# Optimization experiments

Hardware: AMD Instinct MI355X
Metric: run time of the kernel (lower is better)

## Reference

```python
import jax, jax.numpy as jnp
import numpy as np

K = 3
STRIDE = 1
PAD = 1
GROUPS = 16
EPS = 1e-5


def _conv2d(x, w, b, stride, pad):
    out = jax.lax.conv_general_dilated(
        x, w, (stride, stride), [(pad, pad), (pad, pad)],
        dimension_numbers=("NCHW", "OIHW", "NCHW"))
    return out + b[None, :, None, None]


def setup_inputs() -> dict:
    key = jax.random.key(0)
    ks = jax.random.split(key, 6)
    B, Cin, H, W = 4, 256, 64, 64
    Cout = 256
    x = jax.random.normal(ks[0], (B, Cin, H, W), dtype=jnp.float32)
    # DCNv2 offset/mask-generating conv: 3*K*K = 27 output channels
    w_off = jax.random.normal(ks[1], (3 * K * K, Cin, K, K), dtype=jnp.float32) * 0.01
    b_off = jnp.zeros((3 * K * K,), dtype=jnp.float32)
    # main deformable conv weight/bias
    weight = jax.random.normal(ks[2], (Cout, Cin, K, K), dtype=jnp.float32) * 0.02
    bias = jnp.zeros((Cout,), dtype=jnp.float32)
    # GroupNorm affine params
    gamma = jnp.ones((Cout,), dtype=jnp.float32)
    beta = jnp.zeros((Cout,), dtype=jnp.float32)
    return {"x": x, "w_off": w_off, "b_off": b_off,
            "weight": weight, "bias": bias, "gamma": gamma, "beta": beta}


def reference(x, w_off, b_off, weight, bias, gamma, beta):
    B, Cin, H, W = x.shape
    Cout = weight.shape[0]
    KK = K * K

    # --- offset/mask branch (DCNv2): 18 offsets + 9 sigmoid masks ---
    om = _conv2d(x, w_off, b_off, STRIDE, PAD)          # [B, 27, Ho, Wo]
    Ho, Wo = om.shape[2], om.shape[3]
    off_y, off_x, m = jnp.split(om, 3, axis=1)          # each [B, 9, Ho, Wo]
    mask = jax.nn.sigmoid(m)

    # --- sampling coordinates: base grid + kernel tap + learned offset ---
    kgy = jnp.repeat(jnp.arange(K, dtype=x.dtype), K)   # [9] row of tap
    kgx = jnp.tile(jnp.arange(K, dtype=x.dtype), K)     # [9] col of tap
    base_y = jnp.arange(Ho, dtype=x.dtype) * STRIDE - PAD
    base_x = jnp.arange(Wo, dtype=x.dtype) * STRIDE - PAD
    py = base_y[None, None, :, None] + kgy[None, :, None, None] + off_y  # [B,9,Ho,Wo]
    px = base_x[None, None, None, :] + kgx[None, :, None, None] + off_x  # [B,9,Ho,Wo]

    # --- bilinear sampling with zero padding outside the image ---
    y0 = jnp.floor(py)
    x0 = jnp.floor(px)
    wy1 = py - y0
    wx1 = px - x0

    def gather(img, yy, xx):
        # img [Cin,H,W], yy/xx [9,Ho,Wo] int -> [Cin,9,Ho,Wo]
        return img[:, yy, xx]

    def corner(yi, xi, wy, wx):
        valid = (yi >= 0) & (yi < H) & (xi >= 0) & (xi < W)
        yc = jnp.clip(yi, 0, H - 1).astype(jnp.int32)
        xc = jnp.clip(xi, 0, W - 1).astype(jnp.int32)
        vals = jax.vmap(gather)(x, yc, xc)               # [B,Cin,9,Ho,Wo]
        w_ = (wy * wx * valid.astype(x.dtype))[:, None]   # [B,1,9,Ho,Wo]
        return vals * w_

    sampled = (corner(y0, x0, (1 - wy1), (1 - wx1))
               + corner(y0, x0 + 1, (1 - wy1), wx1)
               + corner(y0 + 1, x0, wy1, (1 - wx1))
               + corner(y0 + 1, x0 + 1, wy1, wx1))       # [B,Cin,9,Ho,Wo]
    sampled = sampled * mask[:, None]                     # modulation

    # --- conv accumulation over taps and input channels ---
    out = jnp.einsum("bckhw,ock->bohw", sampled,
                     weight.reshape(Cout, Cin, KK)) + bias[None, :, None, None]

    # --- GroupNorm(16, Cout) ---
    og = out.reshape(B, GROUPS, Cout // GROUPS, Ho, Wo)
    mu = og.mean(axis=(2, 3, 4), keepdims=True)
    var = og.var(axis=(2, 3, 4), keepdims=True)
    og = (og - mu) * jax.lax.rsqrt(var + EPS)
    out = og.reshape(B, Cout, Ho, Wo) * gamma[None, :, None, None] + beta[None, :, None, None]
    return out
```

## Files before the change

### kernel.cpp

```cpp
#include <hip/hip_runtime.h>
#include <math.h>

#define CIN   256
#define COUT  256
#define H     64
#define W     64
#define HW    4096
#define KK    9
#define KC    2304
#define NOFF  27
#define B_    4
#define EPS   1e-5f
#define OM3S  (B_ * NOFF * HW)

typedef __attribute__((ext_vector_type(4))) float f32x4;
typedef __attribute__((ext_vector_type(8))) short s16x8;

static __device__ __forceinline__ unsigned short f2bf(float f) {
  unsigned u = __builtin_bit_cast(unsigned, f);
  u += 0x7FFF + ((u >> 16) & 1);
  return (unsigned short)(u >> 16);
}
static __device__ __forceinline__ float bflo(unsigned u) {
  return __builtin_bit_cast(float, u << 16);
}
static __device__ __forceinline__ float bfhi(unsigned u) {
  return __builtin_bit_cast(float, u & 0xffff0000u);
}
static __device__ __forceinline__ unsigned packbf(float lo, float hi) {
  unsigned ul = __builtin_bit_cast(unsigned, lo);
  unsigned uh = __builtin_bit_cast(unsigned, hi);
  ul += 0x7FFF + ((ul >> 16) & 1);
  uh += 0x7FFF + ((uh >> 16) & 1);
  return (ul >> 16) | (uh & 0xffff0000u);
}

__global__ __launch_bounds__(256) void prep_kernel(
    const float* __restrict__ x, const float* __restrict__ w,
    const float* __restrict__ w_off, unsigned short* __restrict__ xT,
    unsigned short* __restrict__ wBf, unsigned short* __restrict__ wOBf,
    float* __restrict__ gstat) {
  int bi = blockIdx.x;
  int t = threadIdx.x;
  if (bi < 256) {
    __shared__ unsigned short tile[64][272];
    int b = bi >> 6, y = bi & 63;
    const float* src = x + (size_t)b * CIN * HW + y * W;
    for (int r = 0; r < 64; ++r) {
      int idx = r * 256 + t;
      int c = idx >> 6, ww = idx & 63;
      tile[ww][c] = f2bf(src[(size_t)c * HW + ww]);
    }
    __syncthreads();
    unsigned short* dst = xT + ((size_t)(b * 64 + y) * 64) * 256;
    for (int r = 0; r < 8; ++r) {
      int idx = r * 2048 + t * 8;
      int ww = idx >> 8, c = idx & 255;
      *(uint4*)(dst + idx) = *(const uint4*)&tile[ww][c];
    }
  } else if (bi < 544) {
    int pkt = (bi - 256) * 256 + t;
    int lane = pkt & 63;
    int tn = (pkt >> 6) & 15;
    int k2 = pkt >> 10;
    int co = tn * 16 + (lane & 15);
    int kb = k2 * 32 + (lane >> 4) * 8;
    unsigned short v[8];
#pragma unroll
    for (int j = 0; j < 8; ++j) {
      int kk = kb + j;
      int kt = kk >> 8, c = kk & 255;
      v[j] = f2bf(w[(co * 256 + c) * 9 + kt]);
    }
    *(uint4*)&wBf[(size_t)pkt * 8] = *(const uint4*)v;
  } else if (bi < 580) {
    int pkt = (bi - 544) * 256 + t;
    int lane = pkt & 63;
    int tn = (pkt >> 6) & 1;
    int k2 = pkt >> 7;
    int oc = tn * 16 + (lane & 15);
    int kb = k2 * 32 + (lane >> 4) * 8;
    unsigned short v[8];
#pragma unroll
    for (int j = 0; j < 8; ++j) {
      int kk = kb + j;
      int kt = kk >> 8, c = kk & 255;
      v[j] = (oc < NOFF) ? f2bf(w_off[(oc * 256 + c) * 9 + kt]) : (unsigned short)0;
    }
    *(uint4*)&wOBf[(size_t)pkt * 8] = *(const uint4*)v;
  } else {
    if (t < 128) gstat[t] = 0.f;
  }
}

__global__ __launch_bounds__(256) void offconv_mfma_kernel(
    const unsigned short* __restrict__ xT, const unsigned short* __restrict__ wOBf,
    float* __restrict__ om3) {
  int bi = blockIdx.x;
  int ts = bi >> 8;
  int row = bi & 255;
  int b = row >> 6, i = row & 63;
  int t = threadIdx.x, lane = t & 63, wv = t >> 6;
  int lr = lane & 15, lq = lane >> 4;
  int p = wv * 16 + lr;
  const unsigned short* xb = xT + (size_t)b * (HW * 256);
  f32x4 acc[2] = {};

  for (int kc = 0; kc < 3; ++kc) {
    int kt = ts * 3 + kc;
    int ky = kt / 3, kx = kt % 3;
    int yy = i - 1 + ky, xx = p - 1 + kx;
    bool ok = ((unsigned)yy < 64u) && ((unsigned)xx < 64u);
    const unsigned short* ap = xb + ((ok ? yy * 64 + xx : 0) << 8) + lq * 8;
#pragma unroll
    for (int c8 = 0; c8 < 8; ++c8) {
      uint4 av = uint4{0, 0, 0, 0};
      if (ok) av = *(const uint4*)(ap + c8 * 32);
      int k2 = kt * 8 + c8;
      s16x8 a = __builtin_bit_cast(s16x8, av);
      s16x8 b0 = *(const s16x8*)(wOBf + ((((k2 * 2 + 0) << 6) | lane) << 3));
      s16x8 b1 = *(const s16x8*)(wOBf + ((((k2 * 2 + 1) << 6) | lane) << 3));
      acc[0] = __builtin_amdgcn_mfma_f32_16x16x32_bf16(a, b0, acc[0], 0, 0, 0);
      acc[1] = __builtin_amdgcn_mfma_f32_16x16x32_bf16(a, b1, acc[1], 0, 0, 0);
    }
  }
#pragma unroll
  for (int tn = 0; tn < 2; ++tn) {
    int oc = tn * 16 + lr;
    if (oc < NOFF) {
      float* ob = om3 + (size_t)ts * OM3S + ((b * NOFF + oc) << 12) + i * 64 + wv * 16;
#pragma unroll
      for (int r = 0; r < 4; ++r) ob[lq * 4 + r] = acc[tn][r];
    }
  }
}

__global__ __launch_bounds__(512, 2) void gemm_fused_kernel(
    const unsigned short* __restrict__ xT, const float* __restrict__ om3,
    const float* __restrict__ b_off, const unsigned short* __restrict__ wBf,
    const float* __restrict__ bias, unsigned short* __restrict__ cvt,
    float* __restrict__ gstat) {
  __shared__ float tapw[64][KK][4];
  __shared__ int   tapc[64][KK][4];
  __shared__ unsigned short At[2][64 * 64];
  int bid = blockIdx.x;
  int mt = ((bid & 7) << 5) | (bid >> 3);
  int m0 = mt * 64;
  int b = m0 >> 12;
  int irow = (m0 & 4095) >> 6;
  int t = threadIdx.x;
  int lane = t & 63, wv = t >> 6;
  int lr = lane & 15, lq = lane >> 4;
  const unsigned short* xb = xT + (size_t)b * (HW * 256);

  for (int idx = t; idx < 64 * KK; idx += 512) {
    int p = idx / KK, k = idx % KK;
    int pix = (m0 & 4095) + p;
    size_t o = (size_t)(b * NOFF) * HW + pix;
    float offy = om3[o + k * HW] + om3[OM3S + o + k * HW] +
                 om3[2 * OM3S + o + k * HW] + b_off[k];
    float offx = om3[o + (9 + k) * HW] + om3[OM3S + o + (9 + k) * HW] +
                 om3[2 * OM3S + o + (9 + k) * HW] + b_off[9 + k];
    float mval = om3[o + (18 + k) * HW] + om3[OM3S + o + (18 + k) * HW] +
                 om3[2 * OM3S + o + (18 + k) * HW] + b_off[18 + k];
    float mask = 1.f / (1.f + __expf(-mval));
    float py = (float)(irow - 1 + k / 3) + offy;
    float px = (float)(p - 1 + k % 3) + offx;
    float y0f = floorf(py), x0f = floorf(px);
    float wy1 = py - y0f, wx1 = px - x0f;
    int y0 = (int)y0f, x0 = (int)x0f;
    bool y0ok = (unsigned)y0 < 64u, y1ok = (unsigned)(y0 + 1) < 64u;
    bool x0ok = (unsigned)x0 < 64u, x1ok = (unsigned)(x0 + 1) < 64u;
    tapw[p][k][0] = (1.f - wy1) * (1.f - wx1) * mask * (float)(y0ok && x0ok);
    tapw[p][k][1] = (1.f - wy1) * wx1 * mask * (float)(y0ok && x1ok);
    tapw[p][k][2] = wy1 * (1.f - wx1) * mask * (float)(y1ok && x0ok);
    tapw[p][k][3] = wy1 * wx1 * mask * (float)(y1ok && x1ok);
    int y0c = min(max(y0, 0), 63), y1c = min(max(y0 + 1, 0), 63);
    int x0c = min(max(x0, 0), 63), x1c = min(max(x0 + 1, 0), 63);
    tapc[p][k][0] = (y0c * 64 + x0c) * 256;
    tapc[p][k][1] = (x1c - x0c) * 256;
    tapc[p][k][2] = (y1c - y0c) * 64 * 256;
    tapc[p][k][3] = 0;
  }
  __syncthreads();

  bool isProd = (wv < 4);
  int p = (t & 255) >> 2, q = t & 3;
  int cw = isProd ? 0 : (wv - 4);
  const unsigned short* bb = wBf + ((size_t)(cw * 4) * 64 + lane) * 8;

  f32x4 acc[4][4] = {};
  s16x8 Bfa[2][4], Bfb[2][4];
  uint4 sG[8];

#define GLOAD(JJ)                                                            \
  {                                                                          \
    int kt_ = (JJ) >> 2, cg_ = (JJ) & 3;                                     \
    int4 tc_ = *(const int4*)&tapc[p][kt_][0];                               \
    const unsigned short* c_ = xb + tc_.x + cg_ * 64 + q * 16;               \
    sG[0] = *(const uint4*)(c_);                                             \
    sG[1] = *(const uint4*)(c_ + 8);                                         \
    sG[2] = *(const uint4*)(c_ + tc_.y);                                     \
    sG[3] = *(const uint4*)(c_ + tc_.y + 8);                                 \
    sG[4] = *(const uint4*)(c_ + tc_.z);                                     \
    sG[5] = *(const uint4*)(c_ + tc_.z + 8);                                 \
    sG[6] = *(const uint4*)(c_ + tc_.z + tc_.y);                             \
    sG[7] = *(const uint4*)(c_ + tc_.z + tc_.y + 8);                         \
  }

#define COMBINE(JJ, BUFI)                                                    \
  {                                                                          \
    int kt_ = (JJ) >> 2;                                                     \
    f32x4 tw_ = *(const f32x4*)&tapw[p][kt_][0];                             \
    _Pragma("unroll") for (int o = 0; o < 2; ++o) {                          \
      const unsigned* a00_ = (const unsigned*)&sG[0 + o];                    \
      const unsigned* a01_ = (const unsigned*)&sG[2 + o];                    \
      const unsigned* a10_ = (const unsigned*)&sG[4 + o];                    \
      const unsigned* a11_ = (const unsigned*)&sG[6 + o];                    \
      uint4 res_;                                                            \
      unsigned* rr_ = (unsigned*)&res_;                                      \
      _Pragma("unroll") for (int u = 0; u < 4; ++u) {                        \
        float lo_ = tw_[0] * bflo(a00_[u]) + tw_[1] * bflo(a01_[u]) +        \
                    tw_[2] * bflo(a10_[u]) + tw_[3] * bflo(a11_[u]);         \
        float hi_ = tw_[0] * bfhi(a00_[u]) + tw_[1] * bfhi(a01_[u]) +        \
                    tw_[2] * bfhi(a10_[u]) + tw_[3] * bfhi(a11_[u]);         \
        rr_[u] = packbf(lo_, hi_);                                           \
      }                                                                      \
      *(uint4*)((char*)At[BUFI] + p * 128 + (((q * 2 + o) ^ (p & 7)) * 16)) = res_; \
    }                                                                        \
  }

#define BISSUE(J, SLOT)                                                      \
  {                                                                          \
    int k2b_ = (J) * 2;                                                      \
    _Pragma("unroll") for (int kh = 0; kh < 2; ++kh)                         \
      _Pragma("unroll") for (int tn = 0; tn < 4; ++tn)                       \
        SLOT[kh][tn] = *(const s16x8*)(bb + (size_t)(k2b_ + kh) * 8192 + tn * 512); \
  }

#define CONSUME(BUFI, SLOT)                                                  \
  {                                                                          \
    const char* buf_ = (const char*)At[BUFI];                                \
    _Pragma("unroll") for (int kh = 0; kh < 2; ++kh) {                       \
      s16x8 af[4];                                                           \
      _Pragma("unroll") for (int tm = 0; tm < 4; ++tm) {                     \
        int r_ = tm * 16 + lr;                                               \
        af[tm] = *(const s16x8*)(buf_ + r_ * 128 + (((kh * 4 + lq) ^ (r_ & 7)) * 16)); \
      }                                                                      \
      __builtin_amdgcn_s_setprio(1);                                         \
      _Pragma("unroll") for (int tm = 0; tm < 4; ++tm)                       \
        _Pragma("unroll") for (int tn = 0; tn < 4; ++tn)                     \
          acc[tm][tn] = __builtin_amdgcn_mfma_f32_16x16x32_bf16(             \
              af[tm], SLOT[kh][tn], acc[tm][tn], 0, 0, 0);                   \
      __builtin_amdgcn_s_setprio(0);                                         \
    }                                                                        \
  }

#define SOFTBAR()                                                            \
  {                                                                          \
    asm volatile("s_waitcnt lgkmcnt(0)" ::: "memory");                       \
    __builtin_amdgcn_sched_barrier(0);                                       \
    __builtin_amdgcn_s_barrier();                                            \
  }

  if (isProd) {
    GLOAD(0);
    COMBINE(0, 0);
    GLOAD(1);
  } else {
    BISSUE(0, Bfa);
    BISSUE(1, Bfb);
  }
  SOFTBAR();

#pragma unroll 1
  for (int k = 0; k < 36; k += 2) {
    if (isProd) {
      COMBINE(k + 1, 1);
      if (k + 2 < 36) GLOAD(k + 2);
    } else {
      CONSUME(0, Bfa);
      if (k + 2 < 36) BISSUE(k + 2, Bfa);
    }
    SOFTBAR();
    if (isProd) {
      if (k + 2 < 36) COMBINE(k + 2, 0);
      if (k + 3 < 36) GLOAD(k + 3);
    } else {
      CONSUME(1, Bfb);
      if (k + 3 < 36) BISSUE(k + 3, Bfb);
    }
    SOFTBAR();
  }

#undef GLOAD
#undef COMBINE
#undef BISSUE
#undef CONSUME
#undef SOFTBAR

  if (!isProd) {
    int poff = m0 & 4095;
#pragma unroll
    for (int tn = 0; tn < 4; ++tn) {
      int co = cw * 64 + tn * 16 + lr;
      float bco = bias[co];
      unsigned short* cvb = cvt + (size_t)(b * COUT + co) * HW + poff;
      float sS = 0.f, qq = 0.f;
#pragma unroll
      for (int tm = 0; tm < 4; ++tm) {
        ushort4 st;
#pragma unroll
        for (int r = 0; r < 4; ++r) {
          float v = acc[tm][tn][r] + bco;
          sS += v;
          qq += v * v;
          ((unsigned short*)&st)[r] = f2bf(v);
        }
        *(ushort4*)(cvb + tm * 16 + lq * 4) = st;
      }
#pragma unroll
      for (int off = 32; off > 0; off >>= 1) {
        sS += __shfl_down(sS, off, 64);
        qq += __shfl_down(qq, off, 64);
      }
      if (lane == 0) {
        int g = co >> 4;
        atomicAdd(&gstat[(b * 16 + g) * 2 + 0], sS);
        atomicAdd(&gstat[(b * 16 + g) * 2 + 1], qq);
      }
    }
  }
}

__global__ __launch_bounds__(256) void gn_apply_kernel(
    const unsigned short* __restrict__ convout, const float* __restrict__ gstat,
    const float* __restrict__ gamma, const float* __restrict__ beta,
    float* __restrict__ out) {
  int vid = blockIdx.x * 256 + threadIdx.x;
  int e = vid * 8;
  int b = e >> 20;
  int c = (e >> 12) & 255;
  int g = c >> 4;
  float S = gstat[(b * 16 + g) * 2 + 0];
  float Q = gstat[(b * 16 + g) * 2 + 1];
  float mu = S * (1.f / 65536.f);
  float var = Q * (1.f / 65536.f) - mu * mu;
  float rs = rsqrtf(var + EPS);
  float a = rs * gamma[c];
  float bb = beta[c] - mu * a;
  uint4 v = *(const uint4*)(convout + e);
  const unsigned* u = (const unsigned*)&v;
  float4 o0, o1;
  o0.x = bflo(u[0]) * a + bb;  o0.y = bfhi(u[0]) * a + bb;
  o0.z = bflo(u[1]) * a + bb;  o0.w = bfhi(u[1]) * a + bb;
  o1.x = bflo(u[2]) * a + bb;  o1.y = bfhi(u[2]) * a + bb;
  o1.z = bflo(u[3]) * a + bb;  o1.w = bfhi(u[3]) * a + bb;
  *(float4*)(out + e) = o0;
  *(float4*)(out + e + 4) = o1;
}

extern "C" void kernel_launch(void* const* d_in, const int* in_sizes, int n_in,
                              void* d_out, int out_size, void* d_ws, size_t ws_size,
                              hipStream_t stream) {
  const float* x      = (const float*)d_in[0];
  const float* w_off  = (const float*)d_in[1];
  const float* b_off  = (const float*)d_in[2];
  const float* weight = (const float*)d_in[3];
  const float* bias   = (const float*)d_in[4];
  const float* gamma  = (const float*)d_in[5];
  const float* beta   = (const float*)d_in[6];
  float* out = (float*)d_out;

  float* om3 = (float*)d_ws;
  unsigned short* xT   = (unsigned short*)(om3 + (size_t)3 * OM3S);
  unsigned short* wBf  = xT + (size_t)B_ * HW * 256;
  unsigned short* wOBf = wBf + (size_t)COUT * KC;
  unsigned short* cvt  = wOBf + (size_t)32 * KC;
  float* gstat = (float*)(cvt + (size_t)B_ * HW * COUT);

  prep_kernel<<<dim3(581), dim3(256), 0, stream>>>(x, weight, w_off, xT, wBf, wOBf, gstat);
  offconv_mfma_kernel<<<dim3(768), dim3(256), 0, stream>>>(xT, wOBf, om3);
  gemm_fused_kernel<<<dim3(256), dim3(512), 0, stream>>>(xT, om3, b_off, wBf, bias, cvt, gstat);
  gn_apply_kernel<<<dim3(2048), dim3(256), 0, stream>>>(cvt, gstat, gamma, beta, out);
}
```

Baseline: 166.7 us.

## Fuse offset/mask conv into main deformable GEMM kernel via shared memory

```diff
diff --git a/kernel.cpp b/kernel.cpp
--- a/kernel.cpp
+++ b/kernel.cpp
@@ -11,7 +11,6 @@
 #define NOFF  27
 #define B_    4
 #define EPS   1e-5f
-#define OM3S  (B_ * NOFF * HW)
 
 typedef __attribute__((ext_vector_type(4))) float f32x4;
 typedef __attribute__((ext_vector_type(8))) short s16x8;
@@ -93,56 +92,15 @@
   }
 }
 
-__global__ __launch_bounds__(256) void offconv_mfma_kernel(
+__global__ __launch_bounds__(512, 1) void gemm_fused_kernel(
     const unsigned short* __restrict__ xT, const unsigned short* __restrict__ wOBf,
-    float* __restrict__ om3) {
-  int bi = blockIdx.x;
-  int ts = bi >> 8;
-  int row = bi & 255;
-  int b = row >> 6, i = row & 63;
-  int t = threadIdx.x, lane = t & 63, wv = t >> 6;
-  int lr = lane & 15, lq = lane >> 4;
-  int p = wv * 16 + lr;
-  const unsigned short* xb = xT + (size_t)b * (HW * 256);
-  f32x4 acc[2] = {};
-
-  for (int kc = 0; kc < 3; ++kc) {
-    int kt = ts * 3 + kc;
-    int ky = kt / 3, kx = kt % 3;
-    int yy = i - 1 + ky, xx = p - 1 + kx;
-    bool ok = ((unsigned)yy < 64u) && ((unsigned)xx < 64u);
-    const unsigned short* ap = xb + ((ok ? yy * 64 + xx : 0) << 8) + lq * 8;
-#pragma unroll
-    for (int c8 = 0; c8 < 8; ++c8) {
-      uint4 av = uint4{0, 0, 0, 0};
-      if (ok) av = *(const uint4*)(ap + c8 * 32);
-      int k2 = kt * 8 + c8;
-      s16x8 a = __builtin_bit_cast(s16x8, av);
-      s16x8 b0 = *(const s16x8*)(wOBf + ((((k2 * 2 + 0) << 6) | lane) << 3));
-      s16x8 b1 = *(const s16x8*)(wOBf + ((((k2 * 2 + 1) << 6) | lane) << 3));
-      acc[0] = __builtin_amdgcn_mfma_f32_16x16x32_bf16(a, b0, acc[0], 0, 0, 0);
-      acc[1] = __builtin_amdgcn_mfma_f32_16x16x32_bf16(a, b1, acc[1], 0, 0, 0);
-    }
-  }
-#pragma unroll
-  for (int tn = 0; tn < 2; ++tn) {
-    int oc = tn * 16 + lr;
-    if (oc < NOFF) {
-      float* ob = om3 + (size_t)ts * OM3S + ((b * NOFF + oc) << 12) + i * 64 + wv * 16;
-#pragma unroll
-      for (int r = 0; r < 4; ++r) ob[lq * 4 + r] = acc[tn][r];
-    }
-  }
-}
-
-__global__ __launch_bounds__(512, 2) void gemm_fused_kernel(
-    const unsigned short* __restrict__ xT, const float* __restrict__ om3,
     const float* __restrict__ b_off, const unsigned short* __restrict__ wBf,
     const float* __restrict__ bias, unsigned short* __restrict__ cvt,
     float* __restrict__ gstat) {
   __shared__ float tapw[64][KK][4];
   __shared__ int   tapc[64][KK][4];
   __shared__ unsigned short At[2][64 * 64];
+  __shared__ float omL[2][NOFF][64];
   int bid = blockIdx.x;
   int mt = ((bid & 7) << 5) | (bid >> 3);
   int m0 = mt * 64;
@@ -153,16 +111,46 @@
   int lr = lane & 15, lq = lane >> 4;
   const unsigned short* xb = xT + (size_t)b * (HW * 256);
 
+  {
+    int rep = wv >> 2, pw = wv & 3;
+    int pcol = pw * 16 + lr;
+    f32x4 oacc[2] = {};
+    int ktlo = rep ? 5 : 0;
+    int kthi = rep ? 9 : 5;
+    for (int kt = ktlo; kt < kthi; ++kt) {
+      int ky = kt / 3, kx = kt % 3;
+      int yy = irow - 1 + ky, xx = pcol - 1 + kx;
+      bool ok = ((unsigned)yy < 64u) && ((unsigned)xx < 64u);
+      const unsigned short* ap = xb + ((ok ? yy * 64 + xx : 0) << 8) + lq * 8;
+#pragma unroll
+      for (int c8 = 0; c8 < 8; ++c8) {
+        uint4 av = uint4{0, 0, 0, 0};
+        if (ok) av = *(const uint4*)(ap + c8 * 32);
+        int k2 = kt * 8 + c8;
+        s16x8 a = __builtin_bit_cast(s16x8, av);
+        s16x8 b0 = *(const s16x8*)(wOBf + ((((k2 * 2 + 0) << 6) | lane) << 3));
+        s16x8 b1 = *(const s16x8*)(wOBf + ((((k2 * 2 + 1) << 6) | lane) << 3));
+        oacc[0] = __builtin_amdgcn_mfma_f32_16x16x32_bf16(a, b0, oacc[0], 0, 0, 0);
+        oacc[1] = __builtin_amdgcn_mfma_f32_16x16x32_bf16(a, b1, oacc[1], 0, 0, 0);
+      }
+    }
+#pragma unroll
+    for (int tn = 0; tn < 2; ++tn) {
+      int oc = tn * 16 + lr;
+      if (oc < NOFF) {
+#pragma unroll
+        for (int r = 0; r < 4; ++r)
+          omL[rep][oc][pw * 16 + lq * 4 + r] = oacc[tn][r];
+      }
+    }
+  }
+  __syncthreads();
+
   for (int idx = t; idx < 64 * KK; idx += 512) {
     int p = idx / KK, k = idx % KK;
-    int pix = (m0 & 4095) + p;
-    size_t o = (size_t)(b * NOFF) * HW + pix;
-    float offy = om3[o + k * HW] + om3[OM3S + o + k * HW] +
-                 om3[2 * OM3S + o + k * HW] + b_off[k];
-    float offx = om3[o + (9 + k) * HW] + om3[OM3S + o + (9 + k) * HW] +
-                 om3[2 * OM3S + o + (9 + k) * HW] + b_off[9 + k];
-    float mval = om3[o + (18 + k) * HW] + om3[OM3S + o + (18 + k) * HW] +
-                 om3[2 * OM3S + o + (18 + k) * HW] + b_off[18 + k];
+    float offy = omL[0][k][p] + omL[1][k][p] + b_off[k];
+    float offx = omL[0][9 + k][p] + omL[1][9 + k][p] + b_off[9 + k];
+    float mval = omL[0][18 + k][p] + omL[1][18 + k][p] + b_off[18 + k];
     float mask = 1.f / (1.f + __expf(-mval));
     float py = (float)(irow - 1 + k / 3) + offy;
     float px = (float)(p - 1 + k % 3) + offx;
@@ -372,15 +360,13 @@
   const float* beta   = (const float*)d_in[6];
   float* out = (float*)d_out;
 
-  float* om3 = (float*)d_ws;
-  unsigned short* xT   = (unsigned short*)(om3 + (size_t)3 * OM3S);
+  unsigned short* xT   = (unsigned short*)d_ws;
   unsigned short* wBf  = xT + (size_t)B_ * HW * 256;
   unsigned short* wOBf = wBf + (size_t)COUT * KC;
   unsigned short* cvt  = wOBf + (size_t)32 * KC;
   float* gstat = (float*)(cvt + (size_t)B_ * HW * COUT);
 
   prep_kernel<<<dim3(581), dim3(256), 0, stream>>>(x, weight, w_off, xT, wBf, wOBf, gstat);
-  offconv_mfma_kernel<<<dim3(768), dim3(256), 0, stream>>>(xT, wOBf, om3);
-  gemm_fused_kernel<<<dim3(256), dim3(512), 0, stream>>>(xT, om3, b_off, wBf, bias, cvt, gstat);
+  gemm_fused_kernel<<<dim3(256), dim3(512), 0, stream>>>(xT, wOBf, b_off, wBf, bias, cvt, gstat);
   gn_apply_kernel<<<dim3(2048), dim3(256), 0, stream>>>(cvt, gstat, gamma, beta, out);
 }
```

New measurement: 163.0 us. -2.2%, faster.
